# Kernel tuning notes

Hardware: AMD Instinct MI355X
Metric: run time of the kernel (lower is better)

The kernel has to match this reference:

```python
import jax, jax.numpy as jnp
import numpy as np
import math

B, L1, L2, NHID, NH, HD = 4, 2048, 2048, 1024, 16, 64


def setup_inputs() -> dict:
    key = jax.random.key(0)
    ks = jax.random.split(key, 8)
    s = 1.0 / math.sqrt(NHID)  # keep activations O(1)
    inp1 = jax.random.normal(ks[0], (B, L1, NHID), dtype=jnp.float32)
    inp2 = jax.random.normal(ks[1], (B, L2, NHID), dtype=jnp.float32)
    mask = jnp.zeros((B, L2), dtype=bool)
    Wq = jax.random.normal(ks[2], (NHID, NH * HD), dtype=jnp.float32) * s
    Wk = jax.random.normal(ks[3], (NHID, NH * HD), dtype=jnp.float32) * s
    Wv = jax.random.normal(ks[4], (NHID, NH * HD), dtype=jnp.float32) * s
    Wo = jax.random.normal(ks[5], (NH * HD, NHID), dtype=jnp.float32) * s
    bq = jnp.zeros((NH * HD,), jnp.float32)
    bk = jnp.zeros((NH * HD,), jnp.float32)
    bv = jnp.zeros((NH * HD,), jnp.float32)
    bo = jnp.zeros((NHID,), jnp.float32)
    return dict(inp1=inp1, inp2=inp2, mask=mask, Wq=Wq, bq=bq, Wk=Wk, bk=bk,
                Wv=Wv, bv=bv, Wo=Wo, bo=bo)


def reference(inp1, inp2, mask, Wq, bq, Wk, bk, Wv, bv, Wo, bo):
    # q/k/v projections
    q = (inp1 @ Wq + bq) / math.sqrt(HD)              # [B,L1,NH*HD]
    k = inp2 @ Wk + bk                                 # [B,L2,NH*HD]
    v = inp2 @ Wv + bv                                 # [B,L2,NH*HD]
    q = q.reshape(B, L1, NH, HD)
    k = k.reshape(B, L2, NH, HD)
    v = v.reshape(B, L2, NH, HD)
    # scores [B,NH,L1,L2]
    scores = jnp.einsum('bqhd,bkhd->bhqk', q, k)
    scores = jnp.where(mask[:, None, None, :], jnp.float32(-1e8), scores)
    alpha = jax.nn.softmax(scores, axis=-1)
    attn = jnp.einsum('bhqk,bkhd->bqhd', alpha, v).reshape(B, L1, NH * HD)
    return attn @ Wo + bo                              # [B,L1,NHID]
```

## Files before the change

### kernel.cpp

```cpp
#include <hip/hip_runtime.h>
#include <hip/hip_bf16.h>
#include <stdint.h>

using f32x4  = __attribute__((ext_vector_type(4))) float;
using bf16x8 = __attribute__((ext_vector_type(8))) __bf16;

__device__ __forceinline__ unsigned short f2bf(float f) {
  union { float f; unsigned u; } x; x.f = f;
  unsigned r = x.u + 0x7fffu + ((x.u >> 16) & 1u);
  return (unsigned short)(r >> 16);
}

__device__ __forceinline__ void gload_lds16(const void* g, void* l) {
  __builtin_amdgcn_global_load_lds((const __attribute__((address_space(1))) void*)g,
                                   (__attribute__((address_space(3))) void*)l, 16, 0, 0);
}

__global__ __launch_bounds__(256) void f32_to_bf16_k(const float* __restrict__ in,
                                                     unsigned short* __restrict__ out, int n4) {
  int i = blockIdx.x * 256 + threadIdx.x;
  if (i >= n4) return;
  const float4 v = *(const float4*)(in + (size_t)i * 4);
  union { unsigned short s[4]; uint2 u; } p;
  p.s[0] = f2bf(v.x); p.s[1] = f2bf(v.y); p.s[2] = f2bf(v.z); p.s[3] = f2bf(v.w);
  *(uint2*)(out + (size_t)i * 4) = p.u;
}

__global__ __launch_bounds__(256) void prep_wt_k(const float* __restrict__ W,
                                                 unsigned short* __restrict__ WT, float scale) {
  __shared__ float t[32][33];
  const int tx = threadIdx.x & 31, ty = threadIdx.x >> 5;
  const int gx = blockIdx.x * 32, gy = blockIdx.y * 32;
  #pragma unroll
  for (int r = ty; r < 32; r += 8) t[r][tx] = W[(size_t)(gy + r) * 1024 + gx + tx];
  __syncthreads();
  #pragma unroll
  for (int r = ty; r < 32; r += 8)
    WT[(size_t)(gx + r) * 1024 + gy + tx] = f2bf(t[tx][r] * scale);
}

template<int EPI>
__global__ __launch_bounds__(256) void gemm_bt_k(
    const unsigned short* __restrict__ A,
    const unsigned short* __restrict__ BT,
    const float* __restrict__ bias, float bias_scale,
    void* __restrict__ Cv,
    int M, int N, int K) {
  constexpr int BM = 128, BN = 128, BK = 64;
  __shared__ unsigned short sA[BM * BK];
  __shared__ unsigned short sB[BN * BK];
  const int tid = threadIdx.x;
  const int w = tid >> 6, l = tid & 63, l15 = l & 15, lhi = l >> 4;
  const int wr = w >> 1, wc = w & 1;
  const int m0 = blockIdx.y * BM, n0 = blockIdx.x * BN;

  const f32x4 zero = {0.f, 0.f, 0.f, 0.f};
  f32x4 acc[4][4];
  #pragma unroll
  for (int i = 0; i < 4; i++)
    #pragma unroll
    for (int j = 0; j < 4; j++) acc[i][j] = zero;

  for (int k0 = 0; k0 < K; k0 += BK) {
    __syncthreads();
    #pragma unroll
    for (int i = 0; i < 4; i++) {
      const int p = tid + i * 256;
      const int row = p >> 3;
      const int cl = (p & 7) ^ (row & 7);
      gload_lds16(A + (size_t)(m0 + row) * K + k0 + cl * 8, sA + p * 8);
      gload_lds16(BT + (size_t)(n0 + row) * K + k0 + cl * 8, sB + p * 8);
    }
    __syncthreads();
    #pragma unroll
    for (int kk = 0; kk < 2; kk++) {
      bf16x8 af[4], bfr[4];
      #pragma unroll
      for (int mi = 0; mi < 4; mi++) {
        const int row = wr * 64 + mi * 16 + l15;
        const int c = (kk * 4 + lhi) ^ (row & 7);
        af[mi] = *(const bf16x8*)(sA + row * 64 + c * 8);
      }
      #pragma unroll
      for (int ni = 0; ni < 4; ni++) {
        const int row = wc * 64 + ni * 16 + l15;
        const int c = (kk * 4 + lhi) ^ (row & 7);
        bfr[ni] = *(const bf16x8*)(sB + row * 64 + c * 8);
      }
      #pragma unroll
      for (int mi = 0; mi < 4; mi++)
        #pragma unroll
        for (int ni = 0; ni < 4; ni++)
          acc[mi][ni] = __builtin_amdgcn_mfma_f32_16x16x32_bf16(af[mi], bfr[ni], acc[mi][ni], 0, 0, 0);
    }
  }
  #pragma unroll
  for (int mi = 0; mi < 4; mi++) {
    const int gr = m0 + wr * 64 + mi * 16 + lhi * 4;
    #pragma unroll
    for (int ni = 0; ni < 4; ni++) {
      const int gc = n0 + wc * 64 + ni * 16 + l15;
      const float bs = bias[gc] * bias_scale;
      if constexpr (EPI == 0) {
        unsigned short* C = (unsigned short*)Cv;
        #pragma unroll
        for (int j = 0; j < 4; j++)
          C[(size_t)(gr + j) * N + gc] = f2bf(acc[mi][ni][j] + bs);
      } else if constexpr (EPI == 1) {
        unsigned short* C = (unsigned short*)Cv;
        const int bb = gr >> 11, l2 = gr & 2047;
        const int hh = gc >> 6, dd = gc & 63;
        union { unsigned short s[4]; uint2 u; } pk;
        #pragma unroll
        for (int j = 0; j < 4; j++) pk.s[j] = f2bf(acc[mi][ni][j] + bs);
        *(uint2*)(C + ((size_t)((bb * 16 + hh) * 64 + dd) * 2048 + l2)) = pk.u;
      } else {
        float* C = (float*)Cv;
        #pragma unroll
        for (int j = 0; j < 4; j++)
          C[(size_t)(gr + j) * N + gc] = acc[mi][ni][j] + bs;
      }
    }
  }
}

__global__ __launch_bounds__(256, 4) void flash_k(
    const unsigned short* __restrict__ qb,
    const unsigned short* __restrict__ kb,
    const unsigned short* __restrict__ vTb,
    const unsigned char* __restrict__ mask,
    unsigned short* __restrict__ attnb) {
  __shared__ unsigned short sK[2][64 * 64];
  __shared__ unsigned short sV[2][64 * 64];
  __shared__ unsigned short sP[4][16 * 64];
  const int tid = threadIdx.x;
  const int w = tid >> 6, l = tid & 63, l15 = l & 15, lhi = l >> 4;
  const int id = blockIdx.x;
  const int xcd = id & 7;
  const int qt = (id >> 3) & 31;
  const int hb = ((id >> 8) << 3) + xcd;
  const int h = hb & 15, b = hb >> 4;

  const size_t qrow = (size_t)(b * 2048 + qt * 64 + w * 16 + l15);
  const bf16x8 aq0 = *(const bf16x8*)(qb + qrow * 1024 + h * 64 + lhi * 8);
  const bf16x8 aq1 = *(const bf16x8*)(qb + qrow * 1024 + h * 64 + 32 + lhi * 8);

  const f32x4 zero = {0.f, 0.f, 0.f, 0.f};
  f32x4 oacc[5];
  #pragma unroll
  for (int d = 0; d < 5; d++) oacc[d] = zero;
  float mrow[4];
  #pragma unroll
  for (int j = 0; j < 4; j++) mrow[j] = 8.0f;

  bf16x8 onef;
  #pragma unroll
  for (int i = 0; i < 8; i++) onef[i] = (__bf16)1.0f;

  const unsigned short* kbase = kb + (size_t)(b * 2048) * 1024 + h * 64;
  const unsigned short* vbase = vTb + (size_t)((b * 16 + h) * 64) * 2048;
  const unsigned char* mbase = mask + b * 2048;
  unsigned short* sPw = sP[w];

  const int p0 = tid, p1 = tid + 256;
  const int r0 = p0 >> 3, c0s = (p0 & 7) ^ (r0 & 7);
  const int r1 = p1 >> 3, c1s = (p1 & 7) ^ (r1 & 7);
  const unsigned short* kp0 = kbase + (size_t)r0 * 1024 + c0s * 8;
  const unsigned short* kp1 = kbase + (size_t)r1 * 1024 + c1s * 8;
  const unsigned short* vp0 = vbase + (size_t)r0 * 2048 + c0s * 8;
  const unsigned short* vp1 = vbase + (size_t)r1 * 2048 + c1s * 8;

  gload_lds16(kp0, sK[0] + p0 * 8);
  gload_lds16(kp1, sK[0] + p1 * 8);
  gload_lds16(vp0, sV[0] + p0 * 8);
  gload_lds16(vp1, sV[0] + p1 * 8);
  __syncthreads();

  int cur = 0;
  for (int kt = 0; kt < 32; kt++) {
    if (kt < 31) {
      const size_t ko = (size_t)(kt + 1) * 64 * 1024;
      const int vo = (kt + 1) * 64;
      unsigned short* dK = sK[cur ^ 1];
      unsigned short* dV = sV[cur ^ 1];
      gload_lds16(kp0 + ko, dK + p0 * 8);
      gload_lds16(kp1 + ko, dK + p1 * 8);
      gload_lds16(vp0 + vo, dV + p0 * 8);
      gload_lds16(vp1 + vo, dV + p1 * 8);
    }
    const unsigned short* cK = sK[cur];
    const unsigned short* cV = sV[cur];

    f32x4 sacc[4];
    #pragma unroll
    for (int n = 0; n < 4; n++) sacc[n] = zero;
    #pragma unroll
    for (int n = 0; n < 4; n++) {
      const int row = n * 16 + l15;
      const int cc0 = lhi ^ (row & 7);
      const int cc1 = (4 + lhi) ^ (row & 7);
      const bf16x8 b0 = *(const bf16x8*)(cK + row * 64 + cc0 * 8);
      const bf16x8 b1 = *(const bf16x8*)(cK + row * 64 + cc1 * 8);
      sacc[n] = __builtin_amdgcn_mfma_f32_16x16x32_bf16(aq0, b0, sacc[n], 0, 0, 0);
      sacc[n] = __builtin_amdgcn_mfma_f32_16x16x32_bf16(aq1, b1, sacc[n], 0, 0, 0);
    }

    if (__any(mbase[kt * 64 + l] != 0)) {
      #pragma unroll
      for (int n = 0; n < 4; n++) {
        const float mb = mbase[kt * 64 + n * 16 + l15] ? -1e8f : 0.f;
        #pragma unroll
        for (int j = 0; j < 4; j++) sacc[n][j] += mb;
      }
    }

    float lmax[4];
    #pragma unroll
    for (int j = 0; j < 4; j++)
      lmax[j] = fmaxf(fmaxf(sacc[0][j], sacc[1][j]), fmaxf(sacc[2][j], sacc[3][j]));
    const bool need = (lmax[0] > mrow[0]) | (lmax[1] > mrow[1]) |
                      (lmax[2] > mrow[2]) | (lmax[3] > mrow[3]);
    if (__any(need)) {
      float tmax[4] = {lmax[0], lmax[1], lmax[2], lmax[3]};
      #pragma unroll
      for (int d = 1; d < 16; d <<= 1)
        #pragma unroll
        for (int j = 0; j < 4; j++) tmax[j] = fmaxf(tmax[j], __shfl_xor(tmax[j], d));
      #pragma unroll
      for (int j = 0; j < 4; j++) {
        const float mnew = fmaxf(mrow[j], tmax[j]);
        const float scl = exp2f(mrow[j] - mnew);
        mrow[j] = mnew;
        #pragma unroll
        for (int d = 0; d < 5; d++) oacc[d][j] *= scl;
      }
    }

    #pragma unroll
    for (int n = 0; n < 4; n++)
      #pragma unroll
      for (int j = 0; j < 4; j++) {
        const int row = lhi * 4 + j;
        const int col = n * 16 + l15;
        const int cc = (col >> 3) ^ (row & 7);
        *(__bf16*)(sPw + row * 64 + cc * 8 + (col & 7)) =
            (__bf16)exp2f(sacc[n][j] - mrow[j]);
      }
    asm volatile("s_waitcnt lgkmcnt(0)" ::: "memory");
    __builtin_amdgcn_sched_barrier(0);
    {
      const int prow = l15;
      const int pc0 = lhi ^ (prow & 7);
      const int pc1 = (4 + lhi) ^ (prow & 7);
      const bf16x8 pa0 = *(const bf16x8*)(sPw + prow * 64 + pc0 * 8);
      const bf16x8 pa1 = *(const bf16x8*)(sPw + prow * 64 + pc1 * 8);
      #pragma unroll
      for (int df = 0; df < 4; df++) {
        const int row = df * 16 + l15;
        const int cc0 = lhi ^ (row & 7);
        const int cc1 = (4 + lhi) ^ (row & 7);
        const bf16x8 v0 = *(const bf16x8*)(cV + row * 64 + cc0 * 8);
        const bf16x8 v1 = *(const bf16x8*)(cV + row * 64 + cc1 * 8);
        oacc[df] = __builtin_amdgcn_mfma_f32_16x16x32_bf16(pa0, v0, oacc[df], 0, 0, 0);
        oacc[df] = __builtin_amdgcn_mfma_f32_16x16x32_bf16(pa1, v1, oacc[df], 0, 0, 0);
      }
      oacc[4] = __builtin_amdgcn_mfma_f32_16x16x32_bf16(pa0, onef, oacc[4], 0, 0, 0);
      oacc[4] = __builtin_amdgcn_mfma_f32_16x16x32_bf16(pa1, onef, oacc[4], 0, 0, 0);
    }
    __syncthreads();
    cur ^= 1;
  }

  float inv[4];
  #pragma unroll
  for (int j = 0; j < 4; j++) inv[j] = 1.0f / oacc[4][j];
  #pragma unroll
  for (int df = 0; df < 4; df++)
    #pragma unroll
    for (int j = 0; j < 4; j++) {
      const size_t r = (size_t)(b * 2048 + qt * 64 + w * 16 + lhi * 4 + j);
      attnb[r * 1024 + h * 64 + df * 16 + l15] = f2bf(oacc[df][j] * inv[j]);
    }
}

extern "C" void kernel_launch(void* const* d_in, const int* in_sizes, int n_in,
                              void* d_out, int out_size, void* d_ws, size_t ws_size,
                              hipStream_t stream) {
  (void)in_sizes; (void)n_in; (void)out_size; (void)ws_size;
  const float* inp1 = (const float*)d_in[0];
  const float* inp2 = (const float*)d_in[1];
  const unsigned char* mask = (const unsigned char*)d_in[2];
  const float* Wq = (const float*)d_in[3];
  const float* bq = (const float*)d_in[4];
  const float* Wk = (const float*)d_in[5];
  const float* bk = (const float*)d_in[6];
  const float* Wv = (const float*)d_in[7];
  const float* bv = (const float*)d_in[8];
  const float* Wo = (const float*)d_in[9];
  const float* bo = (const float*)d_in[10];
  float* out = (float*)d_out;

  char* p = (char*)d_ws;
  auto alloc = [&](size_t bytes) { char* r = p; p += (bytes + 255) & ~(size_t)255; return r; };
  const size_t ACT = 8192ull * 1024 * 2;
  const size_t WSZ = 1024ull * 1024 * 2;
  unsigned short* x1b  = (unsigned short*)alloc(ACT);
  unsigned short* x2b  = (unsigned short*)alloc(ACT);
  unsigned short* WqT  = (unsigned short*)alloc(WSZ);
  unsigned short* WkT  = (unsigned short*)alloc(WSZ);
  unsigned short* WvT  = (unsigned short*)alloc(WSZ);
  unsigned short* WoT  = (unsigned short*)alloc(WSZ);
  unsigned short* qbuf = (unsigned short*)alloc(ACT);
  unsigned short* kbuf = (unsigned short*)alloc(ACT);
  unsigned short* vTbf = (unsigned short*)alloc(ACT);
  unsigned short* attb = x1b;

  const float QS = 0.18033688011112042f;

  f32_to_bf16_k<<<8192, 256, 0, stream>>>(inp1, x1b, 2097152);
  f32_to_bf16_k<<<8192, 256, 0, stream>>>(inp2, x2b, 2097152);
  dim3 tg(32, 32);
  prep_wt_k<<<tg, 256, 0, stream>>>(Wq, WqT, QS);
  prep_wt_k<<<tg, 256, 0, stream>>>(Wk, WkT, 1.f);
  prep_wt_k<<<tg, 256, 0, stream>>>(Wv, WvT, 1.f);
  prep_wt_k<<<tg, 256, 0, stream>>>(Wo, WoT, 1.f);
  dim3 gg(8, 64);
  gemm_bt_k<0><<<gg, 256, 0, stream>>>(x1b, WqT, bq, QS, qbuf, 8192, 1024, 1024);
  gemm_bt_k<0><<<gg, 256, 0, stream>>>(x2b, WkT, bk, 1.f, kbuf, 8192, 1024, 1024);
  gemm_bt_k<1><<<gg, 256, 0, stream>>>(x2b, WvT, bv, 1.f, vTbf, 8192, 1024, 1024);
  flash_k<<<2048, 256, 0, stream>>>(qbuf, kbuf, vTbf, mask, attb);
  gemm_bt_k<2><<<gg, 256, 0, stream>>>(attb, WoT, bo, 1.f, out, 8192, 1024, 1024);
}
```

Before: 278.1 us.

## Process two query tiles per flash block to reuse K/V tiles

Each flash-attention block now handles 128 query rows: every wave works on two 16-row query groups that share the same K/V tiles loaded into LDS. The grid is halved and launch bounds drop from 4 to 3 blocks per CU. This halves K/V global and LDS traffic per query row and gives each wave more independent MFMA work, at the cost of more registers and lower occupancy. The mask check is also hoisted into a single pre-scan of the whole mask row instead of a per-tile check.

```diff
diff --git a/kernel.cpp b/kernel.cpp
--- a/kernel.cpp
+++ b/kernel.cpp
@@ -124,7 +124,7 @@
   }
 }
 
-__global__ __launch_bounds__(256, 4) void flash_k(
+__global__ __launch_bounds__(256, 3) void flash_k(
     const unsigned short* __restrict__ qb,
     const unsigned short* __restrict__ kb,
     const unsigned short* __restrict__ vTb,
@@ -132,26 +132,29 @@
     unsigned short* __restrict__ attnb) {
   __shared__ unsigned short sK[2][64 * 64];
   __shared__ unsigned short sV[2][64 * 64];
-  __shared__ unsigned short sP[4][16 * 64];
+  __shared__ unsigned short sP[4][2][16 * 64];
   const int tid = threadIdx.x;
   const int w = tid >> 6, l = tid & 63, l15 = l & 15, lhi = l >> 4;
   const int id = blockIdx.x;
   const int xcd = id & 7;
-  const int qt = (id >> 3) & 31;
-  const int hb = ((id >> 8) << 3) + xcd;
+  const int qt = (id >> 3) & 15;
+  const int hb = ((id >> 7) << 3) + xcd;
   const int h = hb & 15, b = hb >> 4;
 
-  const size_t qrow = (size_t)(b * 2048 + qt * 64 + w * 16 + l15);
-  const bf16x8 aq0 = *(const bf16x8*)(qb + qrow * 1024 + h * 64 + lhi * 8);
-  const bf16x8 aq1 = *(const bf16x8*)(qb + qrow * 1024 + h * 64 + 32 + lhi * 8);
+  const size_t qrowA = (size_t)(b * 2048 + qt * 128 + w * 16 + l15);
+  const size_t qrowB = qrowA + 64;
+  const bf16x8 aqA0 = *(const bf16x8*)(qb + qrowA * 1024 + h * 64 + lhi * 8);
+  const bf16x8 aqA1 = *(const bf16x8*)(qb + qrowA * 1024 + h * 64 + 32 + lhi * 8);
+  const bf16x8 aqB0 = *(const bf16x8*)(qb + qrowB * 1024 + h * 64 + lhi * 8);
+  const bf16x8 aqB1 = *(const bf16x8*)(qb + qrowB * 1024 + h * 64 + 32 + lhi * 8);
 
   const f32x4 zero = {0.f, 0.f, 0.f, 0.f};
-  f32x4 oacc[5];
-  #pragma unroll
-  for (int d = 0; d < 5; d++) oacc[d] = zero;
-  float mrow[4];
-  #pragma unroll
-  for (int j = 0; j < 4; j++) mrow[j] = 8.0f;
+  f32x4 oaccA[5], oaccB[5];
+  #pragma unroll
+  for (int d = 0; d < 5; d++) { oaccA[d] = zero; oaccB[d] = zero; }
+  float mrowA[4], mrowB[4];
+  #pragma unroll
+  for (int j = 0; j < 4; j++) { mrowA[j] = 8.0f; mrowB[j] = 8.0f; }
 
   bf16x8 onef;
   #pragma unroll
@@ -160,7 +163,12 @@
   const unsigned short* kbase = kb + (size_t)(b * 2048) * 1024 + h * 64;
   const unsigned short* vbase = vTb + (size_t)((b * 16 + h) * 64) * 2048;
   const unsigned char* mbase = mask + b * 2048;
-  unsigned short* sPw = sP[w];
+  unsigned short* sPA = sP[w][0];
+  unsigned short* sPB = sP[w][1];
+
+  bool anym_lane = false;
+  for (int i = l; i < 2048; i += 64) anym_lane |= (mbase[i] != 0);
+  const bool anym = __any(anym_lane);
 
   const int p0 = tid, p1 = tid + 256;
   const int r0 = p0 >> 3, c0s = (p0 & 7) ^ (r0 & 7);
@@ -191,48 +199,75 @@
     const unsigned short* cK = sK[cur];
     const unsigned short* cV = sV[cur];
 
-    f32x4 sacc[4];
-    #pragma unroll
-    for (int n = 0; n < 4; n++) sacc[n] = zero;
+    f32x4 sA[4], sB[4];
+    #pragma unroll
+    for (int n = 0; n < 4; n++) { sA[n] = zero; sB[n] = zero; }
     #pragma unroll
     for (int n = 0; n < 4; n++) {
       const int row = n * 16 + l15;
       const int cc0 = lhi ^ (row & 7);
       const int cc1 = (4 + lhi) ^ (row & 7);
-      const bf16x8 b0 = *(const bf16x8*)(cK + row * 64 + cc0 * 8);
-      const bf16x8 b1 = *(const bf16x8*)(cK + row * 64 + cc1 * 8);
-      sacc[n] = __builtin_amdgcn_mfma_f32_16x16x32_bf16(aq0, b0, sacc[n], 0, 0, 0);
-      sacc[n] = __builtin_amdgcn_mfma_f32_16x16x32_bf16(aq1, b1, sacc[n], 0, 0, 0);
-    }
-
-    if (__any(mbase[kt * 64 + l] != 0)) {
+      const bf16x8 k0 = *(const bf16x8*)(cK + row * 64 + cc0 * 8);
+      const bf16x8 k1 = *(const bf16x8*)(cK + row * 64 + cc1 * 8);
+      sA[n] = __builtin_amdgcn_mfma_f32_16x16x32_bf16(aqA0, k0, sA[n], 0, 0, 0);
+      sA[n] = __builtin_amdgcn_mfma_f32_16x16x32_bf16(aqA1, k1, sA[n], 0, 0, 0);
+      sB[n] = __builtin_amdgcn_mfma_f32_16x16x32_bf16(aqB0, k0, sB[n], 0, 0, 0);
+      sB[n] = __builtin_amdgcn_mfma_f32_16x16x32_bf16(aqB1, k1, sB[n], 0, 0, 0);
+    }
+
+    if (anym) {
       #pragma unroll
       for (int n = 0; n < 4; n++) {
         const float mb = mbase[kt * 64 + n * 16 + l15] ? -1e8f : 0.f;
         #pragma unroll
-        for (int j = 0; j < 4; j++) sacc[n][j] += mb;
-      }
-    }
-
-    float lmax[4];
-    #pragma unroll
-    for (int j = 0; j < 4; j++)
-      lmax[j] = fmaxf(fmaxf(sacc[0][j], sacc[1][j]), fmaxf(sacc[2][j], sacc[3][j]));
-    const bool need = (lmax[0] > mrow[0]) | (lmax[1] > mrow[1]) |
-                      (lmax[2] > mrow[2]) | (lmax[3] > mrow[3]);
-    if (__any(need)) {
-      float tmax[4] = {lmax[0], lmax[1], lmax[2], lmax[3]};
-      #pragma unroll
-      for (int d = 1; d < 16; d <<= 1)
-        #pragma unroll
-        for (int j = 0; j < 4; j++) tmax[j] = fmaxf(tmax[j], __shfl_xor(tmax[j], d));
-      #pragma unroll
-      for (int j = 0; j < 4; j++) {
-        const float mnew = fmaxf(mrow[j], tmax[j]);
-        const float scl = exp2f(mrow[j] - mnew);
-        mrow[j] = mnew;
-        #pragma unroll
-        for (int d = 0; d < 5; d++) oacc[d][j] *= scl;
+        for (int j = 0; j < 4; j++) { sA[n][j] += mb; sB[n][j] += mb; }
+      }
+    }
+
+    {
+      float lmax[4];
+      #pragma unroll
+      for (int j = 0; j < 4; j++)
+        lmax[j] = fmaxf(fmaxf(sA[0][j], sA[1][j]), fmaxf(sA[2][j], sA[3][j]));
+      const bool need = (lmax[0] > mrowA[0]) | (lmax[1] > mrowA[1]) |
+                        (lmax[2] > mrowA[2]) | (lmax[3] > mrowA[3]);
+      if (__any(need)) {
+        float tmax[4] = {lmax[0], lmax[1], lmax[2], lmax[3]};
+        #pragma unroll
+        for (int d = 1; d < 16; d <<= 1)
+          #pragma unroll
+          for (int j = 0; j < 4; j++) tmax[j] = fmaxf(tmax[j], __shfl_xor(tmax[j], d));
+        #pragma unroll
+        for (int j = 0; j < 4; j++) {
+          const float mnew = fmaxf(mrowA[j], tmax[j]);
+          const float scl = exp2f(mrowA[j] - mnew);
+          mrowA[j] = mnew;
+          #pragma unroll
+          for (int d = 0; d < 5; d++) oaccA[d][j] *= scl;
+        }
+      }
+    }
+    {
+      float lmax[4];
+      #pragma unroll
+      for (int j = 0; j < 4; j++)
+        lmax[j] = fmaxf(fmaxf(sB[0][j], sB[1][j]), fmaxf(sB[2][j], sB[3][j]));
+      const bool need = (lmax[0] > mrowB[0]) | (lmax[1] > mrowB[1]) |
+                        (lmax[2] > mrowB[2]) | (lmax[3] > mrowB[3]);
+      if (__any(need)) {
+        float tmax[4] = {lmax[0], lmax[1], lmax[2], lmax[3]};
+        #pragma unroll
+        for (int d = 1; d < 16; d <<= 1)
+          #pragma unroll
+          for (int j = 0; j < 4; j++) tmax[j] = fmaxf(tmax[j], __shfl_xor(tmax[j], d));
+        #pragma unroll
+        for (int j = 0; j < 4; j++) {
+          const float mnew = fmaxf(mrowB[j], tmax[j]);
+          const float scl = exp2f(mrowB[j] - mnew);
+          mrowB[j] = mnew;
+          #pragma unroll
+          for (int d = 0; d < 5; d++) oaccB[d][j] *= scl;
+        }
       }
     }
 
@@ -243,8 +278,8 @@
         const int row = lhi * 4 + j;
         const int col = n * 16 + l15;
         const int cc = (col >> 3) ^ (row & 7);
-        *(__bf16*)(sPw + row * 64 + cc * 8 + (col & 7)) =
-            (__bf16)exp2f(sacc[n][j] - mrow[j]);
+        *(__bf16*)(sPA + row * 64 + cc * 8 + (col & 7)) = (__bf16)exp2f(sA[n][j] - mrowA[j]);
+        *(__bf16*)(sPB + row * 64 + cc * 8 + (col & 7)) = (__bf16)exp2f(sB[n][j] - mrowB[j]);
       }
     asm volatile("s_waitcnt lgkmcnt(0)" ::: "memory");
     __builtin_amdgcn_sched_barrier(0);
@@ -252,8 +287,10 @@
       const int prow = l15;
       const int pc0 = lhi ^ (prow & 7);
       const int pc1 = (4 + lhi) ^ (prow & 7);
-      const bf16x8 pa0 = *(const bf16x8*)(sPw + prow * 64 + pc0 * 8);
-      const bf16x8 pa1 = *(const bf16x8*)(sPw + prow * 64 + pc1 * 8);
+      const bf16x8 paA0 = *(const bf16x8*)(sPA + prow * 64 + pc0 * 8);
+      const bf16x8 paA1 = *(const bf16x8*)(sPA + prow * 64 + pc1 * 8);
+      const bf16x8 paB0 = *(const bf16x8*)(sPB + prow * 64 + pc0 * 8);
+      const bf16x8 paB1 = *(const bf16x8*)(sPB + prow * 64 + pc1 * 8);
       #pragma unroll
       for (int df = 0; df < 4; df++) {
         const int row = df * 16 + l15;
@@ -261,25 +298,30 @@
         const int cc1 = (4 + lhi) ^ (row & 7);
         const bf16x8 v0 = *(const bf16x8*)(cV + row * 64 + cc0 * 8);
         const bf16x8 v1 = *(const bf16x8*)(cV + row * 64 + cc1 * 8);
-        oacc[df] = __builtin_amdgcn_mfma_f32_16x16x32_bf16(pa0, v0, oacc[df], 0, 0, 0);
-        oacc[df] = __builtin_amdgcn_mfma_f32_16x16x32_bf16(pa1, v1, oacc[df], 0, 0, 0);
-      }
-      oacc[4] = __builtin_amdgcn_mfma_f32_16x16x32_bf16(pa0, onef, oacc[4], 0, 0, 0);
-      oacc[4] = __builtin_amdgcn_mfma_f32_16x16x32_bf16(pa1, onef, oacc[4], 0, 0, 0);
+        oaccA[df] = __builtin_amdgcn_mfma_f32_16x16x32_bf16(paA0, v0, oaccA[df], 0, 0, 0);
+        oaccA[df] = __builtin_amdgcn_mfma_f32_16x16x32_bf16(paA1, v1, oaccA[df], 0, 0, 0);
+        oaccB[df] = __builtin_amdgcn_mfma_f32_16x16x32_bf16(paB0, v0, oaccB[df], 0, 0, 0);
+        oaccB[df] = __builtin_amdgcn_mfma_f32_16x16x32_bf16(paB1, v1, oaccB[df], 0, 0, 0);
+      }
+      oaccA[4] = __builtin_amdgcn_mfma_f32_16x16x32_bf16(paA0, onef, oaccA[4], 0, 0, 0);
+      oaccA[4] = __builtin_amdgcn_mfma_f32_16x16x32_bf16(paA1, onef, oaccA[4], 0, 0, 0);
+      oaccB[4] = __builtin_amdgcn_mfma_f32_16x16x32_bf16(paB0, onef, oaccB[4], 0, 0, 0);
+      oaccB[4] = __builtin_amdgcn_mfma_f32_16x16x32_bf16(paB1, onef, oaccB[4], 0, 0, 0);
     }
     __syncthreads();
     cur ^= 1;
   }
 
-  float inv[4];
-  #pragma unroll
-  for (int j = 0; j < 4; j++) inv[j] = 1.0f / oacc[4][j];
+  float invA[4], invB[4];
+  #pragma unroll
+  for (int j = 0; j < 4; j++) { invA[j] = 1.0f / oaccA[4][j]; invB[j] = 1.0f / oaccB[4][j]; }
   #pragma unroll
   for (int df = 0; df < 4; df++)
     #pragma unroll
     for (int j = 0; j < 4; j++) {
-      const size_t r = (size_t)(b * 2048 + qt * 64 + w * 16 + lhi * 4 + j);
-      attnb[r * 1024 + h * 64 + df * 16 + l15] = f2bf(oacc[df][j] * inv[j]);
+      const size_t rA = (size_t)(b * 2048 + qt * 128 + w * 16 + lhi * 4 + j);
+      attnb[rA * 1024 + h * 64 + df * 16 + l15] = f2bf(oaccA[df][j] * invA[j]);
+      attnb[(rA + 64) * 1024 + h * 64 + df * 16 + l15] = f2bf(oaccB[df][j] * invB[j]);
     }
 }
 
@@ -328,6 +370,6 @@
   gemm_bt_k<0><<<gg, 256, 0, stream>>>(x1b, WqT, bq, QS, qbuf, 8192, 1024, 1024);
   gemm_bt_k<0><<<gg, 256, 0, stream>>>(x2b, WkT, bk, 1.f, kbuf, 8192, 1024, 1024);
   gemm_bt_k<1><<<gg, 256, 0, stream>>>(x2b, WvT, bv, 1.f, vTbf, 8192, 1024, 1024);
-  flash_k<<<2048, 256, 0, stream>>>(qbuf, kbuf, vTbf, mask, attb);
+  flash_k<<<1024, 256, 0, stream>>>(qbuf, kbuf, vTbf, mask, attb);
   gemm_bt_k<2><<<gg, 256, 0, stream>>>(attb, WoT, bo, 1.f, out, 8192, 1024, 1024);
 }
```

New measurement: 276.4 us. No clear change (-0.6%).
